# Optimization experiments

Hardware: AMD Instinct MI355X
Metric: run time of the kernel (lower is better)

## Reference

```python
import jax, jax.numpy as jnp
import numpy as np
import math

E, H, KH, F = 2048, 32, 8, 8192
HD = E // H          # 64
KV = KH * HD         # 512
B, S = 2, 2048
EPS = 1e-5


def _rope_table(seq_len, head_dim, base=10000.0):
    inv = 1.0 / (base ** (np.arange(0, head_dim, 2, dtype=np.float32) / head_dim))
    t = np.arange(seq_len, dtype=np.float32)
    fr = np.outer(t, inv)                               # [S, HD/2]
    return jnp.asarray(np.stack([np.cos(fr), np.sin(fr)], axis=-1))  # [S, HD/2, 2]


def setup_inputs() -> dict:
    key = jax.random.key(0)
    ks = jax.random.split(key, 8)
    x = jax.random.normal(ks[0], (B, S, E), dtype=jnp.float32)
    attention_mask = jnp.tril(jnp.ones((1, 1, S, S), dtype=bool))  # causal
    freqs_cis = _rope_table(S, HD)                                  # [S, 32, 2]
    sc = 0.02
    w_qkv = jax.random.normal(ks[1], (E + 2 * KV, E), dtype=jnp.float32) * sc
    w_o = jax.random.normal(ks[2], (E, E), dtype=jnp.float32) * sc
    w1 = jax.random.normal(ks[3], (F, E), dtype=jnp.float32) * sc
    w3 = jax.random.normal(ks[4], (F, E), dtype=jnp.float32) * sc
    w2 = jax.random.normal(ks[5], (E, F), dtype=jnp.float32) * sc
    attn_norm_w = jnp.ones((E,), dtype=jnp.float32)
    ff_norm_w = jnp.ones((E,), dtype=jnp.float32)
    return {"x": x, "attention_mask": attention_mask, "freqs_cis": freqs_cis,
            "w_qkv": w_qkv, "w_o": w_o, "w1": w1, "w2": w2, "w3": w3,
            "attn_norm_w": attn_norm_w, "ff_norm_w": ff_norm_w}


def _rmsnorm(x, w):
    xf = x.astype(jnp.float32)
    n = xf * jax.lax.rsqrt(jnp.mean(xf * xf, axis=-1, keepdims=True) + EPS)
    return n.astype(x.dtype) * w


def _apply_rope(x, freqs_cis):
    # x: [B, h, S, HD]; freqs_cis: [S, HD/2, 2] broadcasting over B, h
    xf = x.astype(jnp.float32).reshape(*x.shape[:-1], -1, 2)
    c, s = freqs_cis[..., 0], freqs_cis[..., 1]
    x0, x1 = xf[..., 0], xf[..., 1]
    out = jnp.stack([x0 * c - x1 * s, x1 * c + x0 * s], axis=-1)
    return out.reshape(x.shape).astype(x.dtype)


def reference(x, attention_mask, freqs_cis, w_qkv, w_o, w1, w2, w3, attn_norm_w, ff_norm_w):
    bs, seq = x.shape[:2]
    h = _rmsnorm(x, attn_norm_w)
    qkv = h @ w_qkv.T                                   # [B, S, E + 2*KV]
    q, k, v = jnp.split(qkv, [E, E + KV], axis=-1)
    q = q.reshape(bs, seq, H, HD).transpose(0, 2, 1, 3)   # [B, H, S, HD]
    k = k.reshape(bs, seq, KH, HD).transpose(0, 2, 1, 3)  # [B, KH, S, HD]
    v = v.reshape(bs, seq, KH, HD).transpose(0, 2, 1, 3)
    q = _apply_rope(q, freqs_cis)
    k = _apply_rope(k, freqs_cis)
    rep = H // KH
    k = jnp.repeat(k, rep, axis=1)                        # [B, H, S, HD]
    v = jnp.repeat(v, rep, axis=1)
    score = jnp.einsum('bhqd,bhkd->bhqk', q, k) / math.sqrt(HD)
    score = jnp.where(attention_mask, score, -jnp.inf)
    attn = jax.nn.softmax(score, axis=-1)
    o = jnp.einsum('bhqk,bhkd->bhqd', attn, v)
    o = o.transpose(0, 2, 1, 3).reshape(bs, seq, E) @ w_o.T
    h2 = x + o
    g = _rmsnorm(h2, ff_norm_w)
    ff = (jax.nn.silu(g @ w1.T) * (g @ w3.T)) @ w2.T
    return h2 + ff
```

## Files before the change

kernel.cpp:

```cpp
#include <hip/hip_runtime.h>
#include <hip/hip_bf16.h>
#include <cstdint>
#include <cstddef>

typedef __bf16 bf16;
typedef __bf16 bf16x2 __attribute__((ext_vector_type(2)));
typedef __bf16 bf16x4 __attribute__((ext_vector_type(4)));
typedef __bf16 bf16x8 __attribute__((ext_vector_type(8)));
typedef float f32x4 __attribute__((ext_vector_type(4)));
typedef float f32x16 __attribute__((ext_vector_type(16)));

#define EDIM 2048
#define SEQ  2048
#define BATCH 2
#define NH   32
#define NKV  8
#define HD   64
#define FF   8192
#define NTOK 4096
#define QKVN 3072

__device__ __forceinline__ void gld_lds16(const void* gp, void* lp) {
    __builtin_amdgcn_global_load_lds(
        (__attribute__((address_space(1))) void*)(gp),
        (__attribute__((address_space(3))) void*)(lp), 16, 0, 0);
}

__device__ __forceinline__ void remap_xcd(int& bx, int& by) {
    int gx = gridDim.x, gy = gridDim.y;
    int nwg = gx * gy;
    if (((nwg & 63) | (gx & 7) | (gy & 7)) == 0) {
        int l = bx + gx * by;
        int nl = (l & 7) * (nwg >> 3) + (l >> 3);
        int s = nl >> 6, r = nl & 63;
        int spr = gx >> 3;
        bx = (s % spr) * 8 + (r & 7);
        by = (s / spr) * 8 + (r >> 3);
    }
}

__global__ __launch_bounds__(256)
void cvt_f32_bf16(const float* __restrict__ in, bf16* __restrict__ out, long n4) {
    long i = (long)blockIdx.x * blockDim.x + threadIdx.x;
    long stride = (long)gridDim.x * blockDim.x;
    for (; i < n4; i += stride) {
        float4 v = ((const float4*)in)[i];
        bf16x4 o;
        o[0] = (bf16)v.x; o[1] = (bf16)v.y; o[2] = (bf16)v.z; o[3] = (bf16)v.w;
        ((bf16x4*)out)[i] = o;
    }
}

__global__ __launch_bounds__(256)
void rmsnorm_bf16(const float* __restrict__ x, const float* __restrict__ w,
                  bf16* __restrict__ out) {
    __shared__ float red[4];
    const int row = blockIdx.x;
    const long base = (long)row * EDIM;
    const int t = threadIdx.x;
    float4 v0 = *(const float4*)(x + base + t * 4);
    float4 v1 = *(const float4*)(x + base + 1024 + t * 4);
    float ss = v0.x*v0.x + v0.y*v0.y + v0.z*v0.z + v0.w*v0.w
             + v1.x*v1.x + v1.y*v1.y + v1.z*v1.z + v1.w*v1.w;
    #pragma unroll
    for (int off = 1; off < 64; off <<= 1) ss += __shfl_xor(ss, off, 64);
    if ((t & 63) == 0) red[t >> 6] = ss;
    __syncthreads();
    float tot = red[0] + red[1] + red[2] + red[3];
    float inv = rsqrtf(tot * (1.0f / EDIM) + 1e-5f);
    float4 w0 = *(const float4*)(w + t * 4);
    float4 w1 = *(const float4*)(w + 1024 + t * 4);
    bf16x4 o0, o1;
    o0[0] = (bf16)(v0.x * inv * w0.x); o0[1] = (bf16)(v0.y * inv * w0.y);
    o0[2] = (bf16)(v0.z * inv * w0.z); o0[3] = (bf16)(v0.w * inv * w0.w);
    o1[0] = (bf16)(v1.x * inv * w1.x); o1[1] = (bf16)(v1.y * inv * w1.y);
    o1[2] = (bf16)(v1.z * inv * w1.z); o1[3] = (bf16)(v1.w * inv * w1.w);
    *(bf16x4*)(out + base + t * 4) = o0;
    *(bf16x4*)(out + base + 1024 + t * 4) = o1;
}

template<int EPI>
__global__ __launch_bounds__(256, 4)
void gemm_nt(const bf16* __restrict__ A, const bf16* __restrict__ B,
             void* __restrict__ Cv, const float* __restrict__ res,
             int M, int N, int K) {
    __shared__ bf16 As[128 * 32];
    __shared__ bf16 Bs[128 * 32];
    const int tid = threadIdx.x;
    const int lane = tid & 63;
    const int wave = tid >> 6;
    const int wm = (wave >> 1) * 64;
    const int wn = (wave & 1) * 64;

    int bx = blockIdx.x, by = blockIdx.y;
    remap_xcd(bx, by);
    const int bm = by * 128;
    const int bn = bx * 128;
    const int lrow = lane & 15;
    const int koff = (lane >> 4) * 8;

    f32x4 acc[4][4] = {};

    for (int k0 = 0; k0 < K; k0 += 32) {
        __syncthreads();
        #pragma unroll
        for (int t = 0; t < 2; ++t) {
            int c = tid + t * 256;
            int r = c >> 2;
            int kc = (c & 3) * 8;
            gld_lds16(A + (long)(bm + r) * K + k0 + kc, As + c * 8);
            gld_lds16(B + (long)(bn + r) * K + k0 + kc, Bs + c * 8);
        }
        __syncthreads();
        bf16x8 af[4], bfr[4];
        #pragma unroll
        for (int t = 0; t < 4; ++t) {
            af[t]  = *(const bf16x8*)(As + (wm + t * 16 + lrow) * 32 + koff);
            bfr[t] = *(const bf16x8*)(Bs + (wn + t * 16 + lrow) * 32 + koff);
        }
        #pragma unroll
        for (int i = 0; i < 4; ++i)
            #pragma unroll
            for (int j = 0; j < 4; ++j)
                acc[i][j] = __builtin_amdgcn_mfma_f32_16x16x32_bf16(af[i], bfr[j], acc[i][j], 0, 0, 0);
    }

    const int row0 = bm + wm + (lane >> 4) * 4;
    const int col0 = bn + wn + (lane & 15);
    #pragma unroll
    for (int i = 0; i < 4; ++i) {
        #pragma unroll
        for (int j = 0; j < 4; ++j) {
            int col = col0 + j * 16;
            #pragma unroll
            for (int r = 0; r < 4; ++r) {
                long idx = (long)(row0 + i * 16 + r) * N + col;
                float v = acc[i][j][r];
                if (EPI == 0) {
                    ((float*)Cv)[idx] = v;
                } else if (EPI == 1) {
                    ((bf16*)Cv)[idx] = (bf16)v;
                } else {
                    ((float*)Cv)[idx] = v + res[idx];
                }
            }
        }
    }
}

__global__ __launch_bounds__(256, 2)
void gemm_ff(const bf16* __restrict__ A, const bf16* __restrict__ B1,
             const bf16* __restrict__ B3, bf16* __restrict__ C,
             int M, int N, int K) {
    __shared__ bf16 As[128 * 32];
    __shared__ bf16 B1s[128 * 32];
    __shared__ bf16 B3s[128 * 32];
    const int tid = threadIdx.x;
    const int lane = tid & 63;
    const int wave = tid >> 6;
    const int wm = (wave >> 1) * 64;
    const int wn = (wave & 1) * 64;

    int bx = blockIdx.x, by = blockIdx.y;
    remap_xcd(bx, by);
    const int bm = by * 128;
    const int bn = bx * 128;
    const int lrow = lane & 15;
    const int koff = (lane >> 4) * 8;

    f32x4 accu[4][4] = {};
    f32x4 accv[4][4] = {};

    for (int k0 = 0; k0 < K; k0 += 32) {
        __syncthreads();
        #pragma unroll
        for (int t = 0; t < 2; ++t) {
            int c = tid + t * 256;
            int r = c >> 2;
            int kc = (c & 3) * 8;
            gld_lds16(A  + (long)(bm + r) * K + k0 + kc, As  + c * 8);
            gld_lds16(B1 + (long)(bn + r) * K + k0 + kc, B1s + c * 8);
            gld_lds16(B3 + (long)(bn + r) * K + k0 + kc, B3s + c * 8);
        }
        __syncthreads();
        bf16x8 af[4], b1f[4], b3f[4];
        #pragma unroll
        for (int t = 0; t < 4; ++t) {
            af[t]  = *(const bf16x8*)(As  + (wm + t * 16 + lrow) * 32 + koff);
            b1f[t] = *(const bf16x8*)(B1s + (wn + t * 16 + lrow) * 32 + koff);
            b3f[t] = *(const bf16x8*)(B3s + (wn + t * 16 + lrow) * 32 + koff);
        }
        #pragma unroll
        for (int i = 0; i < 4; ++i)
            #pragma unroll
            for (int j = 0; j < 4; ++j) {
                accu[i][j] = __builtin_amdgcn_mfma_f32_16x16x32_bf16(af[i], b1f[j], accu[i][j], 0, 0, 0);
                accv[i][j] = __builtin_amdgcn_mfma_f32_16x16x32_bf16(af[i], b3f[j], accv[i][j], 0, 0, 0);
            }
    }

    const int row0 = bm + wm + (lane >> 4) * 4;
    const int col0 = bn + wn + (lane & 15);
    #pragma unroll
    for (int i = 0; i < 4; ++i) {
        #pragma unroll
        for (int j = 0; j < 4; ++j) {
            int col = col0 + j * 16;
            #pragma unroll
            for (int r = 0; r < 4; ++r) {
                long idx = (long)(row0 + i * 16 + r) * N + col;
                float u = accu[i][j][r];
                float v = accv[i][j][r];
                float sl = u / (1.0f + __expf(-u));
                C[idx] = (bf16)(sl * v);
            }
        }
    }
}

__global__ __launch_bounds__(256)
void rope_prep(const bf16* __restrict__ qkv, const float* __restrict__ fr,
               bf16* __restrict__ Qo, bf16* __restrict__ Ko) {
    const int row = blockIdx.x;
    const int b = row >> 11, s = row & 2047;
    const int t = threadIdx.x;
    const long rbase = (long)row * QKVN;
    #pragma unroll
    for (int i = 0; i < 4; ++i) {
        int p = t + i * 256;
        int hh = p >> 5, d = p & 31;
        bf16x2 xv = *(const bf16x2*)(qkv + rbase + hh * 64 + 2 * d);
        float x0 = (float)xv[0], x1 = (float)xv[1];
        float2 cs = *(const float2*)(fr + (long)(s * 32 + d) * 2);
        bf16x2 o;
        o[0] = (bf16)((x0 * cs.x - x1 * cs.y) * 0.125f);
        o[1] = (bf16)((x1 * cs.x + x0 * cs.y) * 0.125f);
        *(bf16x2*)(Qo + ((long)(b * NH + hh) * SEQ + s) * HD + 2 * d) = o;
    }
    {
        int kh = t >> 5, d = t & 31;
        bf16x2 xv = *(const bf16x2*)(qkv + rbase + EDIM + kh * 64 + 2 * d);
        float x0 = (float)xv[0], x1 = (float)xv[1];
        float2 cs = *(const float2*)(fr + (long)(s * 32 + d) * 2);
        bf16x2 o;
        o[0] = (bf16)(x0 * cs.x - x1 * cs.y);
        o[1] = (bf16)(x1 * cs.x + x0 * cs.y);
        *(bf16x2*)(Ko + ((long)(b * NKV + kh) * SEQ + s) * HD + 2 * d) = o;
    }
}

__global__ __launch_bounds__(256)
void v_prep(const bf16* __restrict__ qkv, bf16* __restrict__ Vt) {
    __shared__ bf16 tile[64 * 72];
    const int blk = blockIdx.x;
    const int b = blk >> 8;
    const int kvh = (blk >> 5) & 7;
    const int st = blk & 31;
    const int t = threadIdx.x;
    #pragma unroll
    for (int i = 0; i < 2; ++i) {
        int c = t + i * 256;
        int kk = c >> 3, hdo = (c & 7) * 8;
        bf16x8 v = *(const bf16x8*)(qkv + (long)(b * SEQ + st * 64 + kk) * QKVN + 2560 + kvh * 64 + hdo);
        *(bf16x8*)(tile + kk * 72 + hdo) = v;
    }
    __syncthreads();
    const long obase = ((long)(b * NKV + kvh) * 32 + st) * 4096;
    #pragma unroll
    for (int i = 0; i < 2; ++i) {
        int c = t + i * 256;
        int hd = c >> 3, ko = (c & 7) * 8;
        bf16x8 v;
        #pragma unroll
        for (int j = 0; j < 8; ++j) v[j] = tile[(ko + j) * 72 + hd];
        *(bf16x8*)(Vt + obase + hd * 64 + ko) = v;
    }
}

__global__ __launch_bounds__(256, 3)
void attn_fwd(const bf16* __restrict__ Q, const bf16* __restrict__ K,
              const bf16* __restrict__ Vt, bf16* __restrict__ Out) {
    __shared__ bf16 Ps[4][32][40];
    const int tid = threadIdx.x, lane = tid & 63, w = tid >> 6;
    const int bh = blockIdx.x;
    const int qt = blockIdx.y;
    const int b = bh >> 5, h = bh & 31;
    const int kvh = h >> 2;
    const int ql = lane & 31;
    const int hh = lane >> 5;
    const int sw = (ql ^ (ql >> 3)) & 3;
    const int q0 = qt * 128 + w * 32;
    const int qmax = q0 + 31;
    const long qbase  = ((long)(b * NH + h) * SEQ + q0) * HD;
    const long kvbase = ((long)(b * NKV + kvh) * SEQ) * HD;
    bf16* Pw = &Ps[w][0][0];

    bf16x8 qa[4];
    #pragma unroll
    for (int ds = 0; ds < 4; ++ds)
        qa[ds] = *(const bf16x8*)(Q + qbase + (long)ql * HD + ds * 16 + hh * 8);

    f32x16 oacc[2] = {};
    float mi = -1e30f, li = 0.f;

    const int nt64 = qt * 2 + 1 + (w >> 1);
    for (int kt = 0; kt < nt64; ++kt) {
        const bf16* Kt  = K  + kvbase + (long)kt * (64 * HD);
        const bf16* Vtt = Vt + kvbase + (long)kt * 4096;
        bf16x8 ka[2][4], va[2][2][2];
        #pragma unroll
        for (int h2 = 0; h2 < 2; ++h2)
            #pragma unroll
            for (int ds = 0; ds < 4; ++ds)
                ka[h2][ds] = *(const bf16x8*)(Kt + (h2 * 32 + ql) * HD + ds * 16 + hh * 8);
        #pragma unroll
        for (int h2 = 0; h2 < 2; ++h2)
            #pragma unroll
            for (int t = 0; t < 2; ++t)
                #pragma unroll
                for (int c = 0; c < 2; ++c)
                    va[h2][t][c] = *(const bf16x8*)(Vtt + (t * 32 + ql) * 64 + h2 * 32 + c * 16 + hh * 8);
        const bool lastt = (kt == nt64 - 1);
        #pragma unroll
        for (int h2 = 0; h2 < 2; ++h2) {
            if (h2 == 1 && kt * 64 + 32 > qmax) break;
            f32x16 s = {};
            #pragma unroll
            for (int ds = 0; ds < 4; ++ds)
                s = __builtin_amdgcn_mfma_f32_32x32x16_bf16(ka[h2][ds], qa[ds], s, 0, 0, 0);
            if (lastt) {
                #pragma unroll
                for (int r = 0; r < 16; ++r) {
                    int kk = kt * 64 + h2 * 32 + (r & 3) + 8 * (r >> 2) + 4 * hh;
                    if (kk > q0 + ql) s[r] = -1e30f;
                }
            }
            float tmax = s[0];
            #pragma unroll
            for (int r = 1; r < 16; ++r) tmax = fmaxf(tmax, s[r]);
            tmax = fmaxf(tmax, __shfl_xor(tmax, 32, 64));
            if (!__all(tmax <= mi)) {
                float mnew = fmaxf(mi, tmax);
                float alpha = __expf(mi - mnew);
                li *= alpha;
                #pragma unroll
                for (int r = 0; r < 16; ++r) { oacc[0][r] *= alpha; oacc[1][r] *= alpha; }
                mi = mnew;
            }
            float psum = 0.f;
            #pragma unroll
            for (int g2 = 0; g2 < 4; ++g2) {
                bf16x4 pw;
                #pragma unroll
                for (int j = 0; j < 4; ++j) {
                    float p = __expf(s[g2 * 4 + j] - mi);
                    psum += p;
                    pw[j] = (bf16)p;
                }
                *(bf16x4*)(Pw + ql * 40 + ((g2 ^ sw) << 3) + 4 * hh) = pw;
            }
            psum += __shfl_xor(psum, 32, 64);
            li += psum;
            bf16x8 p0 = *(const bf16x8*)(Pw + ql * 40 + ((hh ^ sw) << 3));
            bf16x8 p1 = *(const bf16x8*)(Pw + ql * 40 + (((2 + hh) ^ sw) << 3));
            #pragma unroll
            for (int t = 0; t < 2; ++t) {
                oacc[t] = __builtin_amdgcn_mfma_f32_32x32x16_bf16(va[h2][t][0], p0, oacc[t], 0, 0, 0);
                oacc[t] = __builtin_amdgcn_mfma_f32_32x32x16_bf16(va[h2][t][1], p1, oacc[t], 0, 0, 0);
            }
        }
    }

    float inv = 1.0f / li;
    const long obase = ((long)b * SEQ + q0 + ql) * EDIM + h * 64;
    #pragma unroll
    for (int t = 0; t < 2; ++t)
        #pragma unroll
        for (int rg = 0; rg < 4; ++rg) {
            bf16x4 o4;
            #pragma unroll
            for (int j = 0; j < 4; ++j) o4[j] = (bf16)(oacc[t][rg * 4 + j] * inv);
            *(bf16x4*)(Out + obase + t * 32 + rg * 8 + hh * 4) = o4;
        }
}

extern "C" void kernel_launch(void* const* d_in, const int* in_sizes, int n_in,
                              void* d_out, int out_size, void* d_ws, size_t ws_size,
                              hipStream_t stream) {
    const float* x    = (const float*)d_in[0];
    const float* fr   = (const float*)d_in[2];
    const float* wqkv = (const float*)d_in[3];
    const float* wo   = (const float*)d_in[4];
    const float* w1   = (const float*)d_in[5];
    const float* w2   = (const float*)d_in[6];
    const float* w3   = (const float*)d_in[7];
    const float* anw  = (const float*)d_in[8];
    const float* fnw  = (const float*)d_in[9];
    float* out = (float*)d_out;

    const size_t SZ_WQKV = (size_t)QKVN * EDIM;
    const size_t SZ_WO   = (size_t)EDIM * EDIM;
    const size_t SZ_WFF  = (size_t)FF * EDIM;
    const size_t B_WQKV  = SZ_WQKV * 2;
    const size_t B_WO    = SZ_WO * 2;
    const size_t B_WFF   = SZ_WFF * 2;
    const size_t B_HATTN = (size_t)NTOK * EDIM * 2;
    const size_t B_QKV   = (size_t)NTOK * QKVN * 2;
    const size_t B_SCR   = (size_t)NTOK * EDIM * 4;
    const size_t B_FF1   = (size_t)NTOK * FF * 2;
    const size_t NEED = B_WQKV + B_WO + 3 * B_WFF + B_HATTN + B_QKV + B_SCR + B_FF1;
    if (ws_size < NEED) return;

    char* ws = (char*)d_ws;
    size_t off = 0;
    auto alloc = [&](size_t bytes) -> void* {
        void* p = ws + off;
        off += (bytes + 255) & ~(size_t)255;
        return p;
    };
    bf16* wqkv_b = (bf16*)alloc(B_WQKV);
    bf16* wo_b   = (bf16*)alloc(B_WO);
    bf16* w1_b   = (bf16*)alloc(B_WFF);
    bf16* w3_b   = (bf16*)alloc(B_WFF);
    bf16* w2_b   = (bf16*)alloc(B_WFF);
    bf16* h_attn = (bf16*)alloc(B_HATTN);
    bf16* qkv_g  = (bf16*)alloc(B_QKV);
    char* scr    = (char*)alloc(B_SCR);
    bf16* Qb  = (bf16*)scr;
    bf16* Kb  = (bf16*)(scr + (size_t)BATCH * NH * SEQ * HD * 2);
    bf16* Vtb = (bf16*)(scr + (size_t)BATCH * (NH + NKV) * SEQ * HD * 2);
    float* h2 = (float*)scr;
    bf16* ff1 = (bf16*)alloc(B_FF1);
    bf16* g_b = qkv_g;

    cvt_f32_bf16<<<512, 256, 0, stream>>>(wqkv, wqkv_b, (long)(SZ_WQKV / 4));
    cvt_f32_bf16<<<512, 256, 0, stream>>>(wo,   wo_b,   (long)(SZ_WO / 4));
    cvt_f32_bf16<<<512, 256, 0, stream>>>(w1,   w1_b,   (long)(SZ_WFF / 4));
    cvt_f32_bf16<<<512, 256, 0, stream>>>(w3,   w3_b,   (long)(SZ_WFF / 4));
    cvt_f32_bf16<<<512, 256, 0, stream>>>(w2,   w2_b,   (long)(SZ_WFF / 4));
    rmsnorm_bf16<<<NTOK, 256, 0, stream>>>(x, anw, h_attn);
    gemm_nt<1><<<dim3(QKVN / 128, NTOK / 128), 256, 0, stream>>>(
        h_attn, wqkv_b, qkv_g, nullptr, NTOK, QKVN, EDIM);
    rope_prep<<<NTOK, 256, 0, stream>>>(qkv_g, fr, Qb, Kb);
    v_prep<<<BATCH * NKV * (SEQ / 64), 256, 0, stream>>>(qkv_g, Vtb);
    attn_fwd<<<dim3(BATCH * NH, SEQ / 128), 256, 0, stream>>>(Qb, Kb, Vtb, h_attn);
    gemm_nt<2><<<dim3(EDIM / 128, NTOK / 128), 256, 0, stream>>>(
        h_attn, wo_b, h2, x, NTOK, EDIM, EDIM);
    rmsnorm_bf16<<<NTOK, 256, 0, stream>>>(h2, fnw, g_b);
    gemm_ff<<<dim3(FF / 128, NTOK / 128), 256, 0, stream>>>(
        g_b, w1_b, w3_b, ff1, NTOK, FF, EDIM);
    gemm_nt<2><<<dim3(EDIM / 128, NTOK / 128), 256, 0, stream>>>(
        ff1, w2_b, out, h2, NTOK, EDIM, FF);
    (void)in_sizes; (void)n_in; (void)out_size; (void)ws_size;
}
```

Before: 1.079 ms.

## Double GEMM K-tile to 64 with XOR-swizzled LDS layout

```diff
diff --git a/kernel.cpp b/kernel.cpp
--- a/kernel.cpp
+++ b/kernel.cpp
@@ -84,8 +84,8 @@
 void gemm_nt(const bf16* __restrict__ A, const bf16* __restrict__ B,
              void* __restrict__ Cv, const float* __restrict__ res,
              int M, int N, int K) {
-    __shared__ bf16 As[128 * 32];
-    __shared__ bf16 Bs[128 * 32];
+    __shared__ bf16 As[128 * 64];
+    __shared__ bf16 Bs[128 * 64];
     const int tid = threadIdx.x;
     const int lane = tid & 63;
     const int wave = tid >> 6;
@@ -97,32 +97,37 @@
     const int bm = by * 128;
     const int bn = bx * 128;
     const int lrow = lane & 15;
-    const int koff = (lane >> 4) * 8;
+    const int g = lane >> 4;
 
     f32x4 acc[4][4] = {};
 
-    for (int k0 = 0; k0 < K; k0 += 32) {
+    for (int k0 = 0; k0 < K; k0 += 64) {
         __syncthreads();
         #pragma unroll
-        for (int t = 0; t < 2; ++t) {
+        for (int t = 0; t < 4; ++t) {
             int c = tid + t * 256;
-            int r = c >> 2;
-            int kc = (c & 3) * 8;
+            int r = c >> 3;
+            int kc = ((c & 7) ^ (r & 7)) * 8;
             gld_lds16(A + (long)(bm + r) * K + k0 + kc, As + c * 8);
             gld_lds16(B + (long)(bn + r) * K + k0 + kc, Bs + c * 8);
         }
         __syncthreads();
-        bf16x8 af[4], bfr[4];
-        #pragma unroll
-        for (int t = 0; t < 4; ++t) {
-            af[t]  = *(const bf16x8*)(As + (wm + t * 16 + lrow) * 32 + koff);
-            bfr[t] = *(const bf16x8*)(Bs + (wn + t * 16 + lrow) * 32 + koff);
-        }
-        #pragma unroll
-        for (int i = 0; i < 4; ++i)
-            #pragma unroll
-            for (int j = 0; j < 4; ++j)
-                acc[i][j] = __builtin_amdgcn_mfma_f32_16x16x32_bf16(af[i], bfr[j], acc[i][j], 0, 0, 0);
+        #pragma unroll
+        for (int hf = 0; hf < 2; ++hf) {
+            bf16x8 af[4], bfr[4];
+            #pragma unroll
+            for (int t = 0; t < 4; ++t) {
+                int ra = wm + t * 16 + lrow;
+                int rb = wn + t * 16 + lrow;
+                af[t]  = *(const bf16x8*)(As + ra * 64 + ((((hf << 2) + g) ^ (ra & 7)) << 3));
+                bfr[t] = *(const bf16x8*)(Bs + rb * 64 + ((((hf << 2) + g) ^ (rb & 7)) << 3));
+            }
+            #pragma unroll
+            for (int i = 0; i < 4; ++i)
+                #pragma unroll
+                for (int j = 0; j < 4; ++j)
+                    acc[i][j] = __builtin_amdgcn_mfma_f32_16x16x32_bf16(af[i], bfr[j], acc[i][j], 0, 0, 0);
+        }
     }
 
     const int row0 = bm + wm + (lane >> 4) * 4;
@@ -152,9 +157,9 @@
 void gemm_ff(const bf16* __restrict__ A, const bf16* __restrict__ B1,
              const bf16* __restrict__ B3, bf16* __restrict__ C,
              int M, int N, int K) {
-    __shared__ bf16 As[128 * 32];
-    __shared__ bf16 B1s[128 * 32];
-    __shared__ bf16 B3s[128 * 32];
+    __shared__ bf16 As[128 * 64];
+    __shared__ bf16 B1s[128 * 64];
+    __shared__ bf16 B3s[128 * 64];
     const int tid = threadIdx.x;
     const int lane = tid & 63;
     const int wave = tid >> 6;
@@ -166,37 +171,44 @@
     const int bm = by * 128;
     const int bn = bx * 128;
     const int lrow = lane & 15;
-    const int koff = (lane >> 4) * 8;
+    const int g = lane >> 4;
 
     f32x4 accu[4][4] = {};
     f32x4 accv[4][4] = {};
 
-    for (int k0 = 0; k0 < K; k0 += 32) {
+    for (int k0 = 0; k0 < K; k0 += 64) {
         __syncthreads();
         #pragma unroll
-        for (int t = 0; t < 2; ++t) {
+        for (int t = 0; t < 4; ++t) {
             int c = tid + t * 256;
-            int r = c >> 2;
-            int kc = (c & 3) * 8;
+            int r = c >> 3;
+            int kc = ((c & 7) ^ (r & 7)) * 8;
             gld_lds16(A  + (long)(bm + r) * K + k0 + kc, As  + c * 8);
             gld_lds16(B1 + (long)(bn + r) * K + k0 + kc, B1s + c * 8);
             gld_lds16(B3 + (long)(bn + r) * K + k0 + kc, B3s + c * 8);
         }
         __syncthreads();
-        bf16x8 af[4], b1f[4], b3f[4];
-        #pragma unroll
-        for (int t = 0; t < 4; ++t) {
-            af[t]  = *(const bf16x8*)(As  + (wm + t * 16 + lrow) * 32 + koff);
-            b1f[t] = *(const bf16x8*)(B1s + (wn + t * 16 + lrow) * 32 + koff);
-            b3f[t] = *(const bf16x8*)(B3s + (wn + t * 16 + lrow) * 32 + koff);
-        }
-        #pragma unroll
-        for (int i = 0; i < 4; ++i)
-            #pragma unroll
-            for (int j = 0; j < 4; ++j) {
-                accu[i][j] = __builtin_amdgcn_mfma_f32_16x16x32_bf16(af[i], b1f[j], accu[i][j], 0, 0, 0);
-                accv[i][j] = __builtin_amdgcn_mfma_f32_16x16x32_bf16(af[i], b3f[j], accv[i][j], 0, 0, 0);
-            }
+        #pragma unroll
+        for (int hf = 0; hf < 2; ++hf) {
+            bf16x8 af[4], b1f[4], b3f[4];
+            #pragma unroll
+            for (int t = 0; t < 4; ++t) {
+                int ra = wm + t * 16 + lrow;
+                int rb = wn + t * 16 + lrow;
+                int ca = (((hf << 2) + g) ^ (ra & 7)) << 3;
+                int cb = (((hf << 2) + g) ^ (rb & 7)) << 3;
+                af[t]  = *(const bf16x8*)(As  + ra * 64 + ca);
+                b1f[t] = *(const bf16x8*)(B1s + rb * 64 + cb);
+                b3f[t] = *(const bf16x8*)(B3s + rb * 64 + cb);
+            }
+            #pragma unroll
+            for (int i = 0; i < 4; ++i)
+                #pragma unroll
+                for (int j = 0; j < 4; ++j) {
+                    accu[i][j] = __builtin_amdgcn_mfma_f32_16x16x32_bf16(af[i], b1f[j], accu[i][j], 0, 0, 0);
+                    accv[i][j] = __builtin_amdgcn_mfma_f32_16x16x32_bf16(af[i], b3f[j], accv[i][j], 0, 0, 0);
+                }
+        }
     }
 
     const int row0 = bm + wm + (lane >> 4) * 4;
```

Measured after the change: 990.4 us. 8.3% less time.

## Double-buffer LDS tiles in GEMM kernels to overlap global loads with MFMA

Applied to the files above, without the earlier changes.

```diff
diff --git a/kernel.cpp b/kernel.cpp
--- a/kernel.cpp
+++ b/kernel.cpp
@@ -84,8 +84,8 @@
 void gemm_nt(const bf16* __restrict__ A, const bf16* __restrict__ B,
              void* __restrict__ Cv, const float* __restrict__ res,
              int M, int N, int K) {
-    __shared__ bf16 As[128 * 32];
-    __shared__ bf16 Bs[128 * 32];
+    __shared__ bf16 As[2][128 * 32];
+    __shared__ bf16 Bs[2][128 * 32];
     const int tid = threadIdx.x;
     const int lane = tid & 63;
     const int wave = tid >> 6;
@@ -99,30 +99,44 @@
     const int lrow = lane & 15;
     const int koff = (lane >> 4) * 8;
 
+    const int c0 = tid, c1 = tid + 256;
+    const int r0 = c0 >> 2, kc0 = (c0 & 3) * 8;
+    const int r1 = c1 >> 2, kc1 = (c1 & 3) * 8;
+    const bf16* pa0 = A + (long)(bm + r0) * K + kc0;
+    const bf16* pa1 = A + (long)(bm + r1) * K + kc1;
+    const bf16* pb0 = B + (long)(bn + r0) * K + kc0;
+    const bf16* pb1 = B + (long)(bn + r1) * K + kc1;
+
     f32x4 acc[4][4] = {};
 
+    gld_lds16(pa0, &As[0][c0 * 8]);
+    gld_lds16(pa1, &As[0][c1 * 8]);
+    gld_lds16(pb0, &Bs[0][c0 * 8]);
+    gld_lds16(pb1, &Bs[0][c1 * 8]);
+    __syncthreads();
+
+    int buf = 0;
     for (int k0 = 0; k0 < K; k0 += 32) {
-        __syncthreads();
-        #pragma unroll
-        for (int t = 0; t < 2; ++t) {
-            int c = tid + t * 256;
-            int r = c >> 2;
-            int kc = (c & 3) * 8;
-            gld_lds16(A + (long)(bm + r) * K + k0 + kc, As + c * 8);
-            gld_lds16(B + (long)(bn + r) * K + k0 + kc, Bs + c * 8);
-        }
-        __syncthreads();
+        if (k0 + 32 < K) {
+            gld_lds16(pa0 + k0 + 32, &As[buf ^ 1][c0 * 8]);
+            gld_lds16(pa1 + k0 + 32, &As[buf ^ 1][c1 * 8]);
+            gld_lds16(pb0 + k0 + 32, &Bs[buf ^ 1][c0 * 8]);
+            gld_lds16(pb1 + k0 + 32, &Bs[buf ^ 1][c1 * 8]);
+        }
+        __builtin_amdgcn_sched_barrier(0);
         bf16x8 af[4], bfr[4];
         #pragma unroll
         for (int t = 0; t < 4; ++t) {
-            af[t]  = *(const bf16x8*)(As + (wm + t * 16 + lrow) * 32 + koff);
-            bfr[t] = *(const bf16x8*)(Bs + (wn + t * 16 + lrow) * 32 + koff);
+            af[t]  = *(const bf16x8*)(&As[buf][(wm + t * 16 + lrow) * 32 + koff]);
+            bfr[t] = *(const bf16x8*)(&Bs[buf][(wn + t * 16 + lrow) * 32 + koff]);
         }
         #pragma unroll
         for (int i = 0; i < 4; ++i)
             #pragma unroll
             for (int j = 0; j < 4; ++j)
                 acc[i][j] = __builtin_amdgcn_mfma_f32_16x16x32_bf16(af[i], bfr[j], acc[i][j], 0, 0, 0);
+        __syncthreads();
+        buf ^= 1;
     }
 
     const int row0 = bm + wm + (lane >> 4) * 4;
@@ -152,9 +166,9 @@
 void gemm_ff(const bf16* __restrict__ A, const bf16* __restrict__ B1,
              const bf16* __restrict__ B3, bf16* __restrict__ C,
              int M, int N, int K) {
-    __shared__ bf16 As[128 * 32];
-    __shared__ bf16 B1s[128 * 32];
-    __shared__ bf16 B3s[128 * 32];
+    __shared__ bf16 As[2][128 * 32];
+    __shared__ bf16 B1s[2][128 * 32];
+    __shared__ bf16 B3s[2][128 * 32];
     const int tid = threadIdx.x;
     const int lane = tid & 63;
     const int wave = tid >> 6;
@@ -168,27 +182,44 @@
     const int lrow = lane & 15;
     const int koff = (lane >> 4) * 8;
 
+    const int c0 = tid, c1 = tid + 256;
+    const int r0 = c0 >> 2, kc0 = (c0 & 3) * 8;
+    const int r1 = c1 >> 2, kc1 = (c1 & 3) * 8;
+    const bf16* pa0 = A  + (long)(bm + r0) * K + kc0;
+    const bf16* pa1 = A  + (long)(bm + r1) * K + kc1;
+    const bf16* p10 = B1 + (long)(bn + r0) * K + kc0;
+    const bf16* p11 = B1 + (long)(bn + r1) * K + kc1;
+    const bf16* p30 = B3 + (long)(bn + r0) * K + kc0;
+    const bf16* p31 = B3 + (long)(bn + r1) * K + kc1;
+
     f32x4 accu[4][4] = {};
     f32x4 accv[4][4] = {};
 
+    gld_lds16(pa0, &As[0][c0 * 8]);
+    gld_lds16(pa1, &As[0][c1 * 8]);
+    gld_lds16(p10, &B1s[0][c0 * 8]);
+    gld_lds16(p11, &B1s[0][c1 * 8]);
+    gld_lds16(p30, &B3s[0][c0 * 8]);
+    gld_lds16(p31, &B3s[0][c1 * 8]);
+    __syncthreads();
+
+    int buf = 0;
     for (int k0 = 0; k0 < K; k0 += 32) {
-        __syncthreads();
-        #pragma unroll
-        for (int t = 0; t < 2; ++t) {
-            int c = tid + t * 256;
-            int r = c >> 2;
-            int kc = (c & 3) * 8;
-            gld_lds16(A  + (long)(bm + r) * K + k0 + kc, As  + c * 8);
-            gld_lds16(B1 + (long)(bn + r) * K + k0 + kc, B1s + c * 8);
-            gld_lds16(B3 + (long)(bn + r) * K + k0 + kc, B3s + c * 8);
-        }
-        __syncthreads();
+        if (k0 + 32 < K) {
+            gld_lds16(pa0 + k0 + 32, &As[buf ^ 1][c0 * 8]);
+            gld_lds16(pa1 + k0 + 32, &As[buf ^ 1][c1 * 8]);
+            gld_lds16(p10 + k0 + 32, &B1s[buf ^ 1][c0 * 8]);
+            gld_lds16(p11 + k0 + 32, &B1s[buf ^ 1][c1 * 8]);
+            gld_lds16(p30 + k0 + 32, &B3s[buf ^ 1][c0 * 8]);
+            gld_lds16(p31 + k0 + 32, &B3s[buf ^ 1][c1 * 8]);
+        }
+        __builtin_amdgcn_sched_barrier(0);
         bf16x8 af[4], b1f[4], b3f[4];
         #pragma unroll
         for (int t = 0; t < 4; ++t) {
-            af[t]  = *(const bf16x8*)(As  + (wm + t * 16 + lrow) * 32 + koff);
-            b1f[t] = *(const bf16x8*)(B1s + (wn + t * 16 + lrow) * 32 + koff);
-            b3f[t] = *(const bf16x8*)(B3s + (wn + t * 16 + lrow) * 32 + koff);
+            af[t]  = *(const bf16x8*)(&As[buf][(wm + t * 16 + lrow) * 32 + koff]);
+            b1f[t] = *(const bf16x8*)(&B1s[buf][(wn + t * 16 + lrow) * 32 + koff]);
+            b3f[t] = *(const bf16x8*)(&B3s[buf][(wn + t * 16 + lrow) * 32 + koff]);
         }
         #pragma unroll
         for (int i = 0; i < 4; ++i)
@@ -197,6 +228,8 @@
                 accu[i][j] = __builtin_amdgcn_mfma_f32_16x16x32_bf16(af[i], b1f[j], accu[i][j], 0, 0, 0);
                 accv[i][j] = __builtin_amdgcn_mfma_f32_16x16x32_bf16(af[i], b3f[j], accv[i][j], 0, 0, 0);
             }
+        __syncthreads();
+        buf ^= 1;
     }
 
     const int row0 = bm + wm + (lane >> 4) * 4;
```

Result: no change. 1.086 ms (+0.6%).
